# Kernel tuning notes

Measured on AMD Instinct MI355X. Metric: run time of the kernel, lower is better.

The kernel has to match this reference:

```python
import jax, jax.numpy as jnp
import numpy as np

D_MODEL = 128
N_HEADS = 8
RES_SCALE = 2.0 ** (-0.5)  # self_normalizing residual scale

OCC = np.array([65,66,67,68,69,70,71,72,73,74,75,76,77,81,82,83,84,88,89,90,94], dtype=np.int64)


def conv1d_same(x, w, groups=1):
    # x: [B, Cin, T], w: [Cout, Cin//groups, K] -> [B, Cout, T], 'same' padding, no bias
    return jax.lax.conv_general_dilated(
        x, w, window_strides=(1,), padding='SAME',
        dimension_numbers=('NCH', 'OIH', 'NCH'),
        feature_group_count=groups)


def setup_inputs() -> dict:
    key = jax.random.key(0)
    ks = jax.random.split(key, 7)
    B, C, T = 8, 128, 500
    L, D, O, K = 2, D_MODEL, 21, 9
    def lecun(k, shape, fan_in):
        return jax.random.normal(k, shape, dtype=jnp.float32) / jnp.sqrt(jnp.float32(fan_in))
    return {
        'x': jax.random.normal(ks[0], (B, C, T), dtype=jnp.float32),
        'occ_idx': jnp.asarray(OCC),
        'wq': lecun(ks[1], (L, D, O, K), O * K),
        'wk': lecun(ks[2], (L, C * D, 1, K), K),
        'wv': lecun(ks[3], (L, C * D, 1, K), K),
        'wproj': lecun(ks[4], (L, C, D), D),
        'w_head': lecun(ks[5], (40, C * T), C * T),
        'b_head': jnp.zeros((40,), dtype=jnp.float32),
    }


def reference(x, occ_idx, wq, wk, wv, wproj, w_head, b_head):
    B, C, T = x.shape
    L = wq.shape[0]
    H, D = N_HEADS, D_MODEL
    d = D // H  # head dim
    scale = d ** (-0.5)
    selu = jax.nn.selu
    for l in range(L):
        x_occ = x[:, occ_idx]                               # [B, O, T]
        Q = selu(conv1d_same(x_occ, wq[l]))                 # [B, D, T]
        K = selu(conv1d_same(x, wk[l], groups=C))           # [B, C*D, T]
        V = selu(conv1d_same(x, wv[l], groups=C))           # [B, C*D, T]
        Qh = Q.reshape(B, H, d, T)                          # b (h d) t -> b h d t
        Kh = K.reshape(B, C, H, d, T).transpose(0, 2, 1, 3, 4)  # b h c d t
        Vh = V.reshape(B, C, H, d, T).transpose(0, 2, 1, 3, 4)
        gates = selu(jnp.einsum('bhdt,bhcdt->bhct', Qh, Kh) * scale)
        out = jnp.einsum('bhct,bhcdt->bhcdt', gates, Vh)    # [B, H, C, d, T]
        out = out.transpose(0, 2, 1, 3, 4).reshape(B, C, D, T)  # b (c h d) t grouped by c
        # grouped 1x1 conv (groups=C): per-channel projection D -> 1
        out = selu(jnp.einsum('bcdt,cd->bct', out, wproj[l]))
        x = (x + out) * RES_SCALE
    logits = x.reshape(B, -1) @ w_head.T + b_head           # [B, n_classes]
    return logits
```

## Files before the change

### kernel.cpp

```cpp
#include <hip/hip_runtime.h>
#include <math.h>

#define T_LEN   500
#define C_CH    128
#define DM      128
#define N_OCC   21
#define KSZ     9
#define N_OUT   40

typedef _Float16 f16x8 __attribute__((ext_vector_type(8)));
typedef float    f32x16 __attribute__((ext_vector_type(16)));

__device__ __forceinline__ float selu_f(float x) {
    const float lam = 1.0507009873554805f;
    const float la  = 1.7580993408473766f;
    float e   = __expf(x);
    float neg = fmaf(la, e, -la);
    return x > 0.f ? lam * x : neg;
}

__global__ void wq_transpose(const float* __restrict__ wq, float* __restrict__ wqT) {
    int idx = blockIdx.x * 256 + threadIdx.x;
    if (idx >= 2 * N_OCC * KSZ * DM) return;
    int D  = idx & 127;
    int r  = idx >> 7;
    int k  = r % KSZ;
    int r2 = r / KSZ;
    int o  = r2 % N_OCC;
    int l  = r2 / N_OCC;
    wqT[idx] = wq[(((size_t)l * DM + D) * N_OCC + o) * KSZ + k];
}

#define ATCH 4
__global__ __launch_bounds__(128) void qconv_kernel(
    const float* __restrict__ xin, const int* __restrict__ occ,
    const float* __restrict__ wqT, float* __restrict__ qtT, int l)
{
    const int b  = blockIdx.y;
    const int t0 = blockIdx.x * ATCH;
    const int D  = threadIdx.x;
    __shared__ float xo[N_OCC][ATCH + 8];
    for (int i = threadIdx.x; i < N_OCC * (ATCH + 8); i += 128) {
        int o = i / (ATCH + 8), j = i % (ATCH + 8);
        int tg = t0 + j - 4;
        xo[o][j] = (tg >= 0 && tg < T_LEN)
                     ? xin[((size_t)b * C_CH + occ[o]) * T_LEN + tg] : 0.f;
    }
    __syncthreads();

    float acc[ATCH];
#pragma unroll
    for (int tt = 0; tt < ATCH; ++tt) acc[tt] = 0.f;

    for (int o = 0; o < N_OCC; ++o) {
        float xr[ATCH + 8];
#pragma unroll
        for (int j = 0; j < ATCH + 8; ++j) xr[j] = xo[o][j];
#pragma unroll
        for (int k = 0; k < KSZ; ++k) {
            float w = wqT[(((size_t)l * N_OCC + o) * KSZ + k) * DM + D];
#pragma unroll
            for (int tt = 0; tt < ATCH; ++tt)
                acc[tt] = fmaf(xr[tt + k], w, acc[tt]);
        }
    }
    float4 st;
#pragma unroll
    for (int tt = 0; tt < ATCH; ++tt) (&st.x)[tt] = selu_f(acc[tt]);
    *reinterpret_cast<float4*>(&qtT[((size_t)(b * DM + D)) * T_LEN + t0]) = st;
}

__global__ __launch_bounds__(256) void fused_layer(
    const float* __restrict__ xin, const float* __restrict__ qtT,
    const float* __restrict__ wk, const float* __restrict__ wv,
    const float* __restrict__ wproj, float* __restrict__ xout, int l)
{
    const int c = blockIdx.x, b = blockIdx.y, zi = blockIdx.z;
    const int tid  = threadIdx.x;
    const int wave = tid >> 6;
    const int lane = tid & 63;
    const int tcol = lane & 31;
    const int hi   = lane >> 5;

    __shared__ float xs[272];
    const float* xp = xin + ((size_t)(b * C_CH + c)) * T_LEN;
    for (int i = tid; i < 272; i += 256) {
        int tg = zi * 256 + i - 4;
        xs[i] = (tg >= 0 && tg < T_LEN) ? xp[tg] : 0.f;
    }
    __syncthreads();

    f16x8 ak[4], av[4];
#pragma unroll
    for (int ch = 0; ch < 4; ++ch) {
        const int D = ch * 32 + tcol;
        const float* wkp = wk + (((size_t)l * C_CH * DM + (size_t)c * DM + D) * KSZ);
        const float* wvp = wv + (((size_t)l * C_CH * DM + (size_t)c * DM + D) * KSZ);
        if (hi == 0) {
#pragma unroll
            for (int j = 0; j < 8; ++j) {
                ak[ch][j] = (_Float16)wkp[j];
                av[ch][j] = (_Float16)wvp[j];
            }
        } else {
            ak[ch][0] = (_Float16)wkp[8];
            av[ch][0] = (_Float16)wvp[8];
#pragma unroll
            for (int j = 1; j < 8; ++j) {
                ak[ch][j] = (_Float16)0.f;
                av[ch][j] = (_Float16)0.f;
            }
        }
    }

    const float4* wp4p = reinterpret_cast<const float4*>(
        wproj + ((size_t)l * C_CH + c) * DM);

#pragma unroll 1
    for (int ti = 0; ti < 2; ++ti) {
        const int loc0 = wave * 64 + ti * 32;
        const int t    = zi * 256 + loc0 + tcol;
        const int tq   = t < T_LEN ? t : (T_LEN - 1);

        f16x8 bfr;
        {
            const int base = loc0 + tcol + 8 * hi;
#pragma unroll
            for (int j = 0; j < 8; ++j) bfr[j] = (_Float16)xs[base + j];
        }

        float qk[8];
#pragma unroll
        for (int h = 0; h < 8; ++h) qk[h] = 0.f;

#pragma unroll
        for (int ch = 0; ch < 4; ++ch) {
            const float* qTp = qtT + ((size_t)b * DM + ch * 32 + 4 * hi) * T_LEN + tq;
            float qv[16];
#pragma unroll
            for (int I = 0; I < 4; ++I)
#pragma unroll
                for (int i2 = 0; i2 < 4; ++i2)
                    qv[4 * I + i2] = qTp[(size_t)(8 * I + i2) * T_LEN];

            f32x16 acc;
#pragma unroll
            for (int j = 0; j < 16; ++j) acc[j] = 0.f;
            acc = __builtin_amdgcn_mfma_f32_32x32x16_f16(ak[ch], bfr, acc, 0, 0, 0);

            float pA = 0.f, pB = 0.f;
#pragma unroll
            for (int I = 0; I < 4; ++I) {
#pragma unroll
                for (int i2 = 0; i2 < 4; ++i2) {
                    float kv = selu_f(acc[4 * I + i2]);
                    float qvv = qv[4 * I + i2];
                    if (I < 2) pA = fmaf(qvv, kv, pA);
                    else       pB = fmaf(qvv, kv, pB);
                }
            }
            qk[ch * 2 + 0] += pA;
            qk[ch * 2 + 1] += pB;
        }

        float g[8];
#pragma unroll
        for (int h = 0; h < 8; ++h) {
            float full = qk[h] + __shfl_xor(qk[h], 32);
            g[h] = selu_f(full * 0.25f);
        }

        float outp = 0.f;
#pragma unroll
        for (int ch = 0; ch < 4; ++ch) {
            f32x16 acc;
#pragma unroll
            for (int j = 0; j < 16; ++j) acc[j] = 0.f;
            acc = __builtin_amdgcn_mfma_f32_32x32x16_f16(av[ch], bfr, acc, 0, 0, 0);
            float sA = 0.f, sB = 0.f;
#pragma unroll
            for (int I = 0; I < 4; ++I) {
                float4 wq4 = wp4p[ch * 8 + 2 * I + hi];
#pragma unroll
                for (int i2 = 0; i2 < 4; ++i2) {
                    float vv = selu_f(acc[4 * I + i2]);
                    if (I < 2) sA = fmaf((&wq4.x)[i2], vv, sA);
                    else       sB = fmaf((&wq4.x)[i2], vv, sB);
                }
            }
            outp = fmaf(g[ch * 2 + 0], sA, outp);
            outp = fmaf(g[ch * 2 + 1], sB, outp);
        }
        float outf = outp + __shfl_xor(outp, 32);

        if (hi == 0 && t < T_LEN) {
            const float rs = 0.70710678118654752f;
            xout[((size_t)(b * C_CH + c)) * T_LEN + t]
                = (xs[loc0 + tcol + 4] + selu_f(outf)) * rs;
        }
    }
}

#define NCHUNK 8
#define CHUNK  (C_CH * T_LEN / NCHUNK)
__global__ __launch_bounds__(256) void head_partial(
    const float* __restrict__ x, const float* __restrict__ wh,
    float* __restrict__ part)
{
    const int o  = blockIdx.x;
    const int ch = blockIdx.y;
    const int base = ch * CHUNK;
    const float4* wp = reinterpret_cast<const float4*>(wh + (size_t)o * (C_CH * T_LEN) + base);

    float acc[8];
#pragma unroll
    for (int b = 0; b < 8; ++b) acc[b] = 0.f;

    for (int i = threadIdx.x; i < CHUNK / 4; i += 256) {
        float4 w4 = wp[i];
#pragma unroll
        for (int b = 0; b < 8; ++b) {
            float4 x4 = reinterpret_cast<const float4*>(
                x + (size_t)b * (C_CH * T_LEN) + base)[i];
            acc[b] = fmaf(x4.x, w4.x, acc[b]);
            acc[b] = fmaf(x4.y, w4.y, acc[b]);
            acc[b] = fmaf(x4.z, w4.z, acc[b]);
            acc[b] = fmaf(x4.w, w4.w, acc[b]);
        }
    }

#pragma unroll
    for (int b = 0; b < 8; ++b)
#pragma unroll
        for (int off = 32; off > 0; off >>= 1)
            acc[b] += __shfl_down(acc[b], off);

    __shared__ float red[4][8];
    const int lane = threadIdx.x & 63, wid = threadIdx.x >> 6;
    if (lane == 0)
#pragma unroll
        for (int b = 0; b < 8; ++b) red[wid][b] = acc[b];
    __syncthreads();
    if (threadIdx.x < 8) {
        int b = threadIdx.x;
        part[((size_t)o * NCHUNK + ch) * 8 + b]
            = red[0][b] + red[1][b] + red[2][b] + red[3][b];
    }
}

__global__ __launch_bounds__(320) void head_final(
    const float* __restrict__ part, const float* __restrict__ bh,
    float* __restrict__ out)
{
    int i = threadIdx.x;
    if (i >= N_OUT * 8) return;
    int o = i >> 3, b = i & 7;
    float s = bh[o];
#pragma unroll
    for (int ch = 0; ch < NCHUNK; ++ch)
        s += part[((size_t)o * NCHUNK + ch) * 8 + b];
    out[b * N_OUT + o] = s;
}

extern "C" void kernel_launch(void* const* d_in, const int* in_sizes, int n_in,
                              void* d_out, int out_size, void* d_ws, size_t ws_size,
                              hipStream_t stream) {
    const float* x     = (const float*)d_in[0];
    const int*   occ   = (const int*)  d_in[1];
    const float* wq    = (const float*)d_in[2];
    const float* wk    = (const float*)d_in[3];
    const float* wv    = (const float*)d_in[4];
    const float* wproj = (const float*)d_in[5];
    const float* wh    = (const float*)d_in[6];
    const float* bh    = (const float*)d_in[7];
    float* out = (float*)d_out;

    float* ws  = (float*)d_ws;
    float* wqT = ws;
    float* qtb = wqT + 2 * N_OCC * KSZ * DM;
    float* xb0 = qtb + (size_t)8 * T_LEN * DM;
    float* xb1 = xb0 + (size_t)8 * C_CH * T_LEN;
    float* hp  = xb1 + (size_t)8 * C_CH * T_LEN;

    wq_transpose<<<dim3(189), 256, 0, stream>>>(wq, wqT);

    qconv_kernel<<<dim3(125, 8), 128, 0, stream>>>(x, occ, wqT, qtb, 0);
    fused_layer <<<dim3(128, 8, 2), 256, 0, stream>>>(x, qtb, wk, wv, wproj, xb0, 0);

    qconv_kernel<<<dim3(125, 8), 128, 0, stream>>>(xb0, occ, wqT, qtb, 1);
    fused_layer <<<dim3(128, 8, 2), 256, 0, stream>>>(xb0, qtb, wk, wv, wproj, xb1, 1);

    head_partial<<<dim3(N_OUT, NCHUNK), 256, 0, stream>>>(xb1, wh, hp);
    head_final  <<<dim3(1), 320, 0, stream>>>(hp, bh, out);
}
```

Baseline: 136.0 us.

## Prepack fp16 K/V weights, tile Q layout, fold log2e into weights for exp2 SELU

Adds a prep kernel that converts the K/V depthwise weights into fp16 MFMA fragment order, so each fused_layer block loads them with single vector loads instead of scalar strided loads and conversions. The Q output is rewritten in 32-wide time tiles so per-lane Q reads stay within a small contiguous tile, which removes the clamp. SELU arguments are pre-scaled by log2(e), folded into the weights, so the native exp2 instruction can replace expf. In exchange there is an extra prep launch and more workspace, and scaling the weights before fp16 conversion slightly changes rounding.

```diff
diff --git a/kernel.cpp b/kernel.cpp
--- a/kernel.cpp
+++ b/kernel.cpp
@@ -7,16 +7,24 @@
 #define N_OCC   21
 #define KSZ     9
 #define N_OUT   40
+#define LOG2E   1.44269504088896340736f
 
 typedef _Float16 f16x8 __attribute__((ext_vector_type(8)));
 typedef float    f32x16 __attribute__((ext_vector_type(16)));
 
-__device__ __forceinline__ float selu_f(float x) {
-    const float lam = 1.0507009873554805f;
-    const float la  = 1.7580993408473766f;
-    float e   = __expf(x);
-    float neg = fmaf(la, e, -la);
-    return x > 0.f ? lam * x : neg;
+__device__ __forceinline__ float exp2_fast(float y) {
+#if __has_builtin(__builtin_amdgcn_exp2f)
+    return __builtin_amdgcn_exp2f(y);
+#else
+    return exp2f(y);
+#endif
+}
+
+__device__ __forceinline__ float selu2(float y) {
+    const float c1 = 0.7282904300f;
+    const float la = 1.7580993408473766f;
+    float e = exp2_fast(y);
+    return y > 0.f ? c1 * y : fmaf(la, e, -la);
 }
 
 __global__ void wq_transpose(const float* __restrict__ wq, float* __restrict__ wqT) {
@@ -28,13 +36,34 @@
     int r2 = r / KSZ;
     int o  = r2 % N_OCC;
     int l  = r2 / N_OCC;
-    wqT[idx] = wq[(((size_t)l * DM + D) * N_OCC + o) * KSZ + k];
+    wqT[idx] = wq[(((size_t)l * DM + D) * N_OCC + o) * KSZ + k] * LOG2E;
+}
+
+__global__ void wprep_kernel(const float* __restrict__ wk, const float* __restrict__ wv,
+                             _Float16* __restrict__ wkh, _Float16* __restrict__ wvh)
+{
+    int idx = blockIdx.x * 256 + threadIdx.x;
+    if (idx >= 2 * C_CH * 4 * 64) return;
+    int lane = idx & 63;
+    int ch   = (idx >> 6) & 3;
+    int c    = (idx >> 8) & 127;
+    int l    = idx >> 15;
+    int tcol = lane & 31, hi = lane >> 5;
+    int D    = ch * 32 + tcol;
+    const float* wkp = wk + ((size_t)l * C_CH * DM + (size_t)c * DM + D) * KSZ;
+    const float* wvp = wv + ((size_t)l * C_CH * DM + (size_t)c * DM + D) * KSZ;
+#pragma unroll
+    for (int j = 0; j < 8; ++j) {
+        int k = 8 * hi + j;
+        wkh[(size_t)idx * 8 + j] = (k < KSZ) ? (_Float16)(wkp[k] * LOG2E) : (_Float16)0.f;
+        wvh[(size_t)idx * 8 + j] = (k < KSZ) ? (_Float16)(wvp[k] * LOG2E) : (_Float16)0.f;
+    }
 }
 
 #define ATCH 4
 __global__ __launch_bounds__(128) void qconv_kernel(
     const float* __restrict__ xin, const int* __restrict__ occ,
-    const float* __restrict__ wqT, float* __restrict__ qtT, int l)
+    const float* __restrict__ wqT, float* __restrict__ qtT2, int l)
 {
     const int b  = blockIdx.y;
     const int t0 = blockIdx.x * ATCH;
@@ -66,13 +95,15 @@
     }
     float4 st;
 #pragma unroll
-    for (int tt = 0; tt < ATCH; ++tt) (&st.x)[tt] = selu_f(acc[tt]);
-    *reinterpret_cast<float4*>(&qtT[((size_t)(b * DM + D)) * T_LEN + t0]) = st;
+    for (int tt = 0; tt < ATCH; ++tt) (&st.x)[tt] = selu2(acc[tt]);
+    const int tile = t0 >> 5, tl = t0 & 31;
+    *reinterpret_cast<float4*>(
+        &qtT2[((size_t)(b * 16 + tile) * DM + D) * 32 + tl]) = st;
 }
 
 __global__ __launch_bounds__(256) void fused_layer(
-    const float* __restrict__ xin, const float* __restrict__ qtT,
-    const float* __restrict__ wk, const float* __restrict__ wv,
+    const float* __restrict__ xin, const float* __restrict__ qtT2,
+    const f16x8* __restrict__ wkh, const f16x8* __restrict__ wvh,
     const float* __restrict__ wproj, float* __restrict__ xout, int l)
 {
     const int c = blockIdx.x, b = blockIdx.y, zi = blockIdx.z;
@@ -90,27 +121,13 @@
     }
     __syncthreads();
 
+    const f16x8* wkf = wkh + ((size_t)(l * C_CH + c) * 4) * 64 + lane;
+    const f16x8* wvf = wvh + ((size_t)(l * C_CH + c) * 4) * 64 + lane;
     f16x8 ak[4], av[4];
 #pragma unroll
     for (int ch = 0; ch < 4; ++ch) {
-        const int D = ch * 32 + tcol;
-        const float* wkp = wk + (((size_t)l * C_CH * DM + (size_t)c * DM + D) * KSZ);
-        const float* wvp = wv + (((size_t)l * C_CH * DM + (size_t)c * DM + D) * KSZ);
-        if (hi == 0) {
-#pragma unroll
-            for (int j = 0; j < 8; ++j) {
-                ak[ch][j] = (_Float16)wkp[j];
-                av[ch][j] = (_Float16)wvp[j];
-            }
-        } else {
-            ak[ch][0] = (_Float16)wkp[8];
-            av[ch][0] = (_Float16)wvp[8];
-#pragma unroll
-            for (int j = 1; j < 8; ++j) {
-                ak[ch][j] = (_Float16)0.f;
-                av[ch][j] = (_Float16)0.f;
-            }
-        }
+        ak[ch] = wkf[ch * 64];
+        av[ch] = wvf[ch * 64];
     }
 
     const float4* wp4p = reinterpret_cast<const float4*>(
@@ -119,8 +136,8 @@
 #pragma unroll 1
     for (int ti = 0; ti < 2; ++ti) {
         const int loc0 = wave * 64 + ti * 32;
+        const int tile = zi * 8 + wave * 2 + ti;
         const int t    = zi * 256 + loc0 + tcol;
-        const int tq   = t < T_LEN ? t : (T_LEN - 1);
 
         f16x8 bfr;
         {
@@ -135,13 +152,14 @@
 
 #pragma unroll
         for (int ch = 0; ch < 4; ++ch) {
-            const float* qTp = qtT + ((size_t)b * DM + ch * 32 + 4 * hi) * T_LEN + tq;
+            const float* qTp = qtT2
+                + ((size_t)(b * 16 + tile) * DM + ch * 32 + 4 * hi) * 32 + tcol;
             float qv[16];
 #pragma unroll
             for (int I = 0; I < 4; ++I)
 #pragma unroll
                 for (int i2 = 0; i2 < 4; ++i2)
-                    qv[4 * I + i2] = qTp[(size_t)(8 * I + i2) * T_LEN];
+                    qv[4 * I + i2] = qTp[(8 * I + i2) * 32];
 
             f32x16 acc;
 #pragma unroll
@@ -153,7 +171,7 @@
             for (int I = 0; I < 4; ++I) {
 #pragma unroll
                 for (int i2 = 0; i2 < 4; ++i2) {
-                    float kv = selu_f(acc[4 * I + i2]);
+                    float kv = selu2(acc[4 * I + i2]);
                     float qvv = qv[4 * I + i2];
                     if (I < 2) pA = fmaf(qvv, kv, pA);
                     else       pB = fmaf(qvv, kv, pB);
@@ -167,7 +185,7 @@
 #pragma unroll
         for (int h = 0; h < 8; ++h) {
             float full = qk[h] + __shfl_xor(qk[h], 32);
-            g[h] = selu_f(full * 0.25f);
+            g[h] = selu2(full * (0.25f * LOG2E));
         }
 
         float outp = 0.f;
@@ -183,7 +201,7 @@
                 float4 wq4 = wp4p[ch * 8 + 2 * I + hi];
 #pragma unroll
                 for (int i2 = 0; i2 < 4; ++i2) {
-                    float vv = selu_f(acc[4 * I + i2]);
+                    float vv = selu2(acc[4 * I + i2]);
                     if (I < 2) sA = fmaf((&wq4.x)[i2], vv, sA);
                     else       sB = fmaf((&wq4.x)[i2], vv, sB);
                 }
@@ -196,7 +214,7 @@
         if (hi == 0 && t < T_LEN) {
             const float rs = 0.70710678118654752f;
             xout[((size_t)(b * C_CH + c)) * T_LEN + t]
-                = (xs[loc0 + tcol + 4] + selu_f(outf)) * rs;
+                = (xs[loc0 + tcol + 4] + selu2(outf * LOG2E)) * rs;
         }
     }
 }
@@ -278,17 +296,22 @@
     float* ws  = (float*)d_ws;
     float* wqT = ws;
     float* qtb = wqT + 2 * N_OCC * KSZ * DM;
-    float* xb0 = qtb + (size_t)8 * T_LEN * DM;
+    float* xb0 = qtb + (size_t)8 * 16 * DM * 32;
     float* xb1 = xb0 + (size_t)8 * C_CH * T_LEN;
     float* hp  = xb1 + (size_t)8 * C_CH * T_LEN;
+    _Float16* wkh = (_Float16*)(hp + N_OUT * NCHUNK * 8);
+    _Float16* wvh = wkh + (size_t)2 * C_CH * 4 * 64 * 8;
 
     wq_transpose<<<dim3(189), 256, 0, stream>>>(wq, wqT);
+    wprep_kernel<<<dim3(256), 256, 0, stream>>>(wk, wv, wkh, wvh);
 
     qconv_kernel<<<dim3(125, 8), 128, 0, stream>>>(x, occ, wqT, qtb, 0);
-    fused_layer <<<dim3(128, 8, 2), 256, 0, stream>>>(x, qtb, wk, wv, wproj, xb0, 0);
+    fused_layer <<<dim3(128, 8, 2), 256, 0, stream>>>(
+        x, qtb, (const f16x8*)wkh, (const f16x8*)wvh, wproj, xb0, 0);
 
     qconv_kernel<<<dim3(125, 8), 128, 0, stream>>>(xb0, occ, wqT, qtb, 1);
-    fused_layer <<<dim3(128, 8, 2), 256, 0, stream>>>(xb0, qtb, wk, wv, wproj, xb1, 1);
+    fused_layer <<<dim3(128, 8, 2), 256, 0, stream>>>(
+        xb0, qtb, (const f16x8*)wkh, (const f16x8*)wvh, wproj, xb1, 1);
 
     head_partial<<<dim3(N_OUT, NCHUNK), 256, 0, stream>>>(xb1, wh, hp);
     head_final  <<<dim3(1), 320, 0, stream>>>(hp, bh, out);
```

Measured after the change: 129.0 us. 1.05x faster.
